# Kernel tuning notes

Measured on AMD Instinct MI355X. Metric: run time of the kernel, lower is better.

The kernel has to match this reference:

```python
import jax, jax.numpy as jnp
import numpy as np

B, S, D_IN, D_OUT, R = 8, 2048, 2048, 2048, 16

def setup_inputs() -> dict:
    key = jax.random.key(0)
    k = jax.random.split(key, 5)
    scale_w = 1.0 / np.sqrt(D_IN)
    return {
        "x": jax.random.normal(k[0], (B, S, D_IN), dtype=jnp.float32),
        "A_params": jax.random.normal(k[1], (B, D_OUT, R), dtype=jnp.float32) * 0.02,
        "B_params": jax.random.normal(k[2], (B, R, D_IN), dtype=jnp.float32) * 0.02,
        "W": jax.random.normal(k[3], (D_OUT, D_IN), dtype=jnp.float32) * scale_w,
        "b": jax.random.normal(k[4], (D_OUT,), dtype=jnp.float32) * scale_w,
    }

def reference(x, A_params, B_params, W, b):
    # base: x @ W^T + b  -> [B, S, out]
    base_out = jnp.einsum("bsi,oi->bso", x, W) + b
    # intermediate = x @ B^T -> [B, S, r]
    intermediate = jnp.einsum("bsi,bri->bsr", x, B_params)
    # adaptation = intermediate @ A^T -> [B, S, out]
    adaptation = jnp.einsum("bsr,bor->bso", intermediate, A_params)
    return base_out + adaptation
```

## Files before the change

### kernel.cpp

```cpp
#include <hip/hip_runtime.h>
#include <cstdint>
#include <cstddef>

typedef __attribute__((ext_vector_type(4))) float  floatx4;
typedef __attribute__((ext_vector_type(8))) __bf16 bf16x8;
typedef __attribute__((ext_vector_type(8))) unsigned short u16x8;

#define M_TOT 16384
#define N_TOT 2048
#define K_TOT 2048
#define NBATCH 8
#define RLORA 16
#define NT 32

__device__ __forceinline__ unsigned short f32_to_bf16(float f) {
  unsigned u = __float_as_uint(f);
  u += 0x7fffu + ((u >> 16) & 1u);
  return (unsigned short)(u >> 16);
}

#define GLOAD_LDS16(gp, lp)                                                        \
  __builtin_amdgcn_global_load_lds((__attribute__((address_space(1))) void*)(void*)(gp), \
                                   (__attribute__((address_space(3))) void*)(void*)(lp), \
                                   16, 0, 0)

template<int V> struct IC { static constexpr int value = V; };

__global__ void k_convert(const float* __restrict__ in, unsigned short* __restrict__ out, int n8) {
  int i = blockIdx.x * blockDim.x + threadIdx.x;
  if (i >= n8) return;
  const float4* p = (const float4*)in + (size_t)i * 2;
  float4 v0 = p[0], v1 = p[1];
  u16x8 o;
  o[0] = f32_to_bf16(v0.x); o[1] = f32_to_bf16(v0.y);
  o[2] = f32_to_bf16(v0.z); o[3] = f32_to_bf16(v0.w);
  o[4] = f32_to_bf16(v1.x); o[5] = f32_to_bf16(v1.y);
  o[6] = f32_to_bf16(v1.z); o[7] = f32_to_bf16(v1.w);
  *(u16x8*)(out + (size_t)i * 8) = o;
}

__global__ void k_convert_a(const float* __restrict__ A, unsigned short* __restrict__ abf) {
  int row = blockIdx.x * blockDim.x + threadIdx.x;
  if (row >= NBATCH * N_TOT) return;
  const float4* p = (const float4*)(A + (size_t)row * RLORA);
  float4 v0 = p[0], v1 = p[1], v2 = p[2], v3 = p[3];
  u16x8 lo, hi2, z = {0,0,0,0,0,0,0,0};
  lo[0] = f32_to_bf16(v0.x); lo[1] = f32_to_bf16(v0.y);
  lo[2] = f32_to_bf16(v0.z); lo[3] = f32_to_bf16(v0.w);
  lo[4] = f32_to_bf16(v1.x); lo[5] = f32_to_bf16(v1.y);
  lo[6] = f32_to_bf16(v1.z); lo[7] = f32_to_bf16(v1.w);
  hi2[0] = f32_to_bf16(v2.x); hi2[1] = f32_to_bf16(v2.y);
  hi2[2] = f32_to_bf16(v2.z); hi2[3] = f32_to_bf16(v2.w);
  hi2[4] = f32_to_bf16(v3.x); hi2[5] = f32_to_bf16(v3.y);
  hi2[6] = f32_to_bf16(v3.z); hi2[7] = f32_to_bf16(v3.w);
  u16x8* dst = (u16x8*)(abf + (size_t)row * 32);
  dst[0] = lo; dst[1] = hi2; dst[2] = z; dst[3] = z;
}

__global__ __launch_bounds__(256) void k_inter(const unsigned short* __restrict__ xbf,
                                               const unsigned short* __restrict__ bpbf,
                                               unsigned short* __restrict__ interbf) {
  const int tid  = threadIdx.x;
  const int lane = tid & 63;
  const int wv   = tid >> 6;
  const int l15  = lane & 15;
  const int hi   = lane >> 4;
  const int m0   = blockIdx.x * 64;
  const int bb   = m0 >> 11;

  floatx4 zero = {0.f, 0.f, 0.f, 0.f};
  floatx4 acc[4] = {zero, zero, zero, zero};

  const unsigned short* bpb = bpbf + (size_t)bb * (RLORA * K_TOT);
  const int kb0 = wv * 512;
  for (int kb = kb0; kb < kb0 + 512; kb += 32) {
    bf16x8 bfr = *(const bf16x8*)(bpb + (size_t)l15 * K_TOT + kb + hi * 8);
    #pragma unroll
    for (int mi = 0; mi < 4; ++mi) {
      bf16x8 afr = *(const bf16x8*)(xbf + (size_t)(m0 + mi * 16 + l15) * K_TOT + kb + hi * 8);
      acc[mi] = __builtin_amdgcn_mfma_f32_16x16x32_bf16(afr, bfr, acc[mi], 0, 0, 0);
    }
  }

  __shared__ floatx4 red[4][4][64];
  #pragma unroll
  for (int mi = 0; mi < 4; ++mi) red[wv][mi][lane] = acc[mi];
  __syncthreads();
  if (wv == 0) {
    #pragma unroll
    for (int mi = 0; mi < 4; ++mi) {
      floatx4 s = red[0][mi][lane] + red[1][mi][lane] + red[2][mi][lane] + red[3][mi][lane];
      #pragma unroll
      for (int j = 0; j < 4; ++j) {
        int m = m0 + mi * 16 + hi * 4 + j;
        interbf[(size_t)m * 32 + l15] = f32_to_bf16(s[j]);
        interbf[(size_t)m * 32 + 16 + l15] = 0;
      }
    }
  }
}

#define STAGE_A(bufi, h, tt) do {                                                      \
  GLOAD_LDS16(Ag + (h)*262144 + (tt)*64 + gOff0, AsB + ((bufi)*2+(h))*16384 + ldsB0);  \
  GLOAD_LDS16(Ag + (h)*262144 + (tt)*64 + gOff1, AsB + ((bufi)*2+(h))*16384 + ldsB1);  \
} while(0)
#define STAGE_B(bufi, h, tt) do {                                                      \
  GLOAD_LDS16(Bg + (h)*262144 + (tt)*64 + gOff0, BsB + ((bufi)*2+(h))*16384 + ldsB0);  \
  GLOAD_LDS16(Bg + (h)*262144 + (tt)*64 + gOff1, BsB + ((bufi)*2+(h))*16384 + ldsB1);  \
} while(0)
#define RDA_(B2, qm, mi, ks) (*(const bf16x8*)(AsB + (B2)*32768 + aBase + (qm)*8192 + (mi)*2048 + koff[ks]))
#define RDB_(B2, ni, ks)     (*(const bf16x8*)(BsB + (B2)*32768 + bBase + (ni)*2048 + koff[ks]))
#define BAR() __builtin_amdgcn_s_barrier()
#define MFMA16(MB, NB, AF, BF) do {                                                        \
  _Pragma("unroll")                                                                        \
  for (int mi = 0; mi < 4; ++mi) {                                                         \
    _Pragma("unroll")                                                                      \
    for (int j = 0; j < 2; ++j) {                                                          \
      acc[(MB)+mi][(NB)+j] = __builtin_amdgcn_mfma_f32_16x16x32_bf16(AF[mi][0], BF[j][0], acc[(MB)+mi][(NB)+j], 0, 0, 0); \
      acc[(MB)+mi][(NB)+j] = __builtin_amdgcn_mfma_f32_16x16x32_bf16(AF[mi][1], BF[j][1], acc[(MB)+mi][(NB)+j], 0, 0, 0); \
    }                                                                                      \
  }                                                                                        \
} while(0)

__global__ __launch_bounds__(512, 2) void k_gemm(const unsigned short* __restrict__ xbf,
                                                 const unsigned short* __restrict__ wbf,
                                                 const unsigned short* __restrict__ interbf,
                                                 const unsigned short* __restrict__ abf,
                                                 const float* __restrict__ bias,
                                                 float* __restrict__ out) {
  __shared__ unsigned short As[2][2][8192];
  __shared__ unsigned short Bs[2][2][8192];
  const int tid  = threadIdx.x;
  const int lane = tid & 63;
  const int wid  = tid >> 6;
  const int wm   = wid >> 2;
  const int wn   = wid & 3;
  const int l15  = lane & 15;
  const int hi   = lane >> 4;
  const int swz  = l15 & 7;

  int bid  = blockIdx.x;
  int swzb = ((bid & 7) << 6) | (bid >> 3);
  const int mt = swzb >> 3;
  const int nt = swzb & 7;
  const int mrow0 = mt << 8;
  const int ncol0 = nt << 8;
  const int bb = mrow0 >> 11;

  const int m0 = mrow0 + wm * 128;
  const int n0 = ncol0 + wn * 64;

  const unsigned short* Ag = xbf + (size_t)mrow0 * K_TOT;
  const unsigned short* Bg = wbf + (size_t)ncol0 * K_TOT;
  char* AsB = (char*)As;
  char* BsB = (char*)Bs;

  const int r0    = tid >> 3;
  const int k80   = (tid & 7) ^ (r0 & 7);
  const int gOff0 = r0 * K_TOT + k80 * 8;
  const int gOff1 = gOff0 + 64 * K_TOT;
  const int ldsB0 = wid * 1024;
  const int ldsB1 = 8192 + wid * 1024;

  const int aBase = wm * 16384 + l15 * 128;
  const int bBase = wn * 8192  + l15 * 128;
  int koff[2];
  koff[0] = ((0 * 4 + hi) ^ swz) * 16;
  koff[1] = ((1 * 4 + hi) ^ swz) * 16;

  floatx4 acc[8][4];
  bf16x8 afA[4][2], afB[4][2], bfP[2][2], bfQ[2][2];

  {
    bf16x8 la[8], lb[4];
    #pragma unroll
    for (int mi = 0; mi < 8; ++mi)
      la[mi] = *(const bf16x8*)(interbf + (size_t)(m0 + mi * 16 + l15) * 32 + hi * 8);
    #pragma unroll
    for (int ni = 0; ni < 4; ++ni)
      lb[ni] = *(const bf16x8*)(abf + ((size_t)bb * N_TOT + n0 + ni * 16 + l15) * 32 + hi * 8);

    STAGE_B(0, 0, 0); STAGE_B(0, 1, 0); STAGE_A(0, 0, 0); STAGE_A(0, 1, 0);
    STAGE_B(1, 0, 1); STAGE_B(1, 1, 1); STAGE_A(1, 0, 1);

    floatx4 z = {0.f, 0.f, 0.f, 0.f};
    #pragma unroll
    for (int mi = 0; mi < 8; ++mi)
      #pragma unroll
      for (int ni = 0; ni < 4; ++ni)
        acc[mi][ni] = __builtin_amdgcn_mfma_f32_16x16x32_bf16(la[mi], lb[ni], z, 0, 0, 0);
  }
  asm volatile("s_waitcnt vmcnt(6)" ::: "memory");
  BAR();
  #pragma unroll
  for (int mi = 0; mi < 4; ++mi) { afA[mi][0] = RDA_(0, 0, mi, 0); afA[mi][1] = RDA_(0, 0, mi, 1); }
  #pragma unroll
  for (int j = 0; j < 2; ++j)    { bfP[j][0]  = RDB_(0, j, 0);     bfP[j][1]  = RDB_(0, j, 1); }

  auto tile_step = [&](int t, auto bufc, auto s1c, auto s2c, auto vmc, auto lastc,
                       auto& bfF, auto& bfS) {
    constexpr int BUF  = decltype(bufc)::value;
    constexpr int S1   = decltype(s1c)::value;
    constexpr int S2   = decltype(s2c)::value;
    constexpr int VM   = decltype(vmc)::value;
    constexpr int LAST = decltype(lastc)::value;

    #pragma unroll
    for (int j = 0; j < 2; ++j) { bfS[j][0] = RDB_(BUF, 2 + j, 0); bfS[j][1] = RDB_(BUF, 2 + j, 1); }
    if constexpr (S1) STAGE_A(BUF ^ 1, 1, t + 1);
    BAR();
    asm volatile("s_waitcnt lgkmcnt(4)" ::: "memory");
    __builtin_amdgcn_s_setprio(1);
    MFMA16(0, 0, afA, bfF);
    __builtin_amdgcn_s_setprio(0);
    BAR();

    #pragma unroll
    for (int mi = 0; mi < 4; ++mi) { afB[mi][0] = RDA_(BUF, 1, mi, 0); afB[mi][1] = RDA_(BUF, 1, mi, 1); }
    BAR();
    asm volatile("s_waitcnt lgkmcnt(8)" ::: "memory");
    __builtin_amdgcn_s_setprio(1);
    MFMA16(0, 2, afA, bfS);
    __builtin_amdgcn_s_setprio(0);
    BAR();

    if constexpr (S2) { STAGE_B(BUF, 0, t + 2); STAGE_B(BUF, 1, t + 2); }
    BAR();
    asm volatile("s_waitcnt lgkmcnt(0)" ::: "memory");
    __builtin_amdgcn_s_setprio(1);
    MFMA16(4, 2, afB, bfS);
    __builtin_amdgcn_s_setprio(0);
    if constexpr (VM == 4)      asm volatile("s_waitcnt vmcnt(4)" ::: "memory");
    else if constexpr (VM == 0) asm volatile("s_waitcnt vmcnt(0)" ::: "memory");
    BAR();

    if constexpr (!LAST) {
      #pragma unroll
      for (int mi = 0; mi < 4; ++mi) { afA[mi][0] = RDA_(BUF ^ 1, 0, mi, 0); afA[mi][1] = RDA_(BUF ^ 1, 0, mi, 1); }
      #pragma unroll
      for (int j = 0; j < 2; ++j)    { bfS[j][0] = RDB_(BUF ^ 1, j, 0);      bfS[j][1] = RDB_(BUF ^ 1, j, 1); }
    }
    if constexpr (S2) STAGE_A(BUF, 0, t + 2);
    BAR();
    __builtin_amdgcn_s_setprio(1);
    MFMA16(4, 0, afB, bfF);
    __builtin_amdgcn_s_setprio(0);
    BAR();
  };

  for (int t = 0; t < NT - 2; t += 2) {
    tile_step(t,     IC<0>{}, IC<1>{}, IC<1>{}, IC<4>{}, IC<0>{}, bfP, bfQ);
    tile_step(t + 1, IC<1>{}, IC<1>{}, IC<1>{}, IC<4>{}, IC<0>{}, bfQ, bfP);
  }
  tile_step(NT - 2, IC<0>{}, IC<1>{}, IC<0>{}, IC<0>{},  IC<0>{}, bfP, bfQ);
  tile_step(NT - 1, IC<1>{}, IC<0>{}, IC<0>{}, IC<-1>{}, IC<1>{}, bfQ, bfP);

  #pragma unroll
  for (int ni = 0; ni < 4; ++ni) {
    int col = n0 + ni * 16 + l15;
    float bv = bias[col];
    #pragma unroll
    for (int mi = 0; mi < 8; ++mi) {
      int r = m0 + mi * 16 + hi * 4;
      #pragma unroll
      for (int j = 0; j < 4; ++j)
        out[(size_t)(r + j) * N_TOT + col] = acc[mi][ni][j] + bv;
    }
  }
}

extern "C" void kernel_launch(void* const* d_in, const int* in_sizes, int n_in,
                              void* d_out, int out_size, void* d_ws, size_t ws_size,
                              hipStream_t stream) {
  const float* x    = (const float*)d_in[0];
  const float* Ap   = (const float*)d_in[1];
  const float* Bp   = (const float*)d_in[2];
  const float* W    = (const float*)d_in[3];
  const float* bias = (const float*)d_in[4];
  float* out = (float*)d_out;

  char* ws = (char*)d_ws;
  unsigned short* xbf     = (unsigned short*)(ws);
  unsigned short* wbf     = (unsigned short*)(ws + 67108864);
  unsigned short* abf     = (unsigned short*)(ws + 67108864 + 8388608);
  unsigned short* bpbf    = (unsigned short*)(ws + 67108864 + 8388608 + 1048576);
  unsigned short* interbf = (unsigned short*)(ws + 67108864 + 8388608 + 1048576 + 524288);

  k_convert<<<dim3(16384), dim3(256), 0, stream>>>(x,  xbf,  4194304);
  k_convert<<<dim3(2048),  dim3(256), 0, stream>>>(W,  wbf,   524288);
  k_convert<<<dim3(128),   dim3(256), 0, stream>>>(Bp, bpbf,   32768);
  k_convert_a<<<dim3(64),  dim3(256), 0, stream>>>(Ap, abf);

  k_inter<<<dim3(256), dim3(256), 0, stream>>>(xbf, bpbf, interbf);

  k_gemm<<<dim3(512), dim3(512), 0, stream>>>(xbf, wbf, interbf, abf, bias, out);
}
```

Measured before the change: 198.8 us.

## Fuse x bf16 conversion into LoRA intermediate kernel and rebalance B-tile prefetch

The separate fp32-to-bf16 conversion passes over x and B_params are folded into the k_inter kernel. It reads fp32 x directly, converts it in registers, feeds the MFMA and writes the bf16 copy for the main GEMM. This removes one full read of x's bf16 copy and two kernel launches. Separately, the main GEMM's tile step now splits the two B-tile global stages and issues the next buffer's B fragment LDS reads earlier, using finer vmcnt waits, to overlap loads with MFMA work. The risk is that k_inter now runs with only 256 blocks while doing the heavy conversion traffic, so bandwidth use may be poor.

```diff
diff --git a/kernel.cpp b/kernel.cpp
--- a/kernel.cpp
+++ b/kernel.cpp
@@ -19,6 +19,15 @@
   return (unsigned short)(u >> 16);
 }
 
+__device__ __forceinline__ u16x8 cvt8(const float4& a, const float4& b) {
+  u16x8 o;
+  o[0] = f32_to_bf16(a.x); o[1] = f32_to_bf16(a.y);
+  o[2] = f32_to_bf16(a.z); o[3] = f32_to_bf16(a.w);
+  o[4] = f32_to_bf16(b.x); o[5] = f32_to_bf16(b.y);
+  o[6] = f32_to_bf16(b.z); o[7] = f32_to_bf16(b.w);
+  return o;
+}
+
 #define GLOAD_LDS16(gp, lp)                                                        \
   __builtin_amdgcn_global_load_lds((__attribute__((address_space(1))) void*)(void*)(gp), \
                                    (__attribute__((address_space(3))) void*)(void*)(lp), \
@@ -30,35 +39,21 @@
   int i = blockIdx.x * blockDim.x + threadIdx.x;
   if (i >= n8) return;
   const float4* p = (const float4*)in + (size_t)i * 2;
-  float4 v0 = p[0], v1 = p[1];
-  u16x8 o;
-  o[0] = f32_to_bf16(v0.x); o[1] = f32_to_bf16(v0.y);
-  o[2] = f32_to_bf16(v0.z); o[3] = f32_to_bf16(v0.w);
-  o[4] = f32_to_bf16(v1.x); o[5] = f32_to_bf16(v1.y);
-  o[6] = f32_to_bf16(v1.z); o[7] = f32_to_bf16(v1.w);
-  *(u16x8*)(out + (size_t)i * 8) = o;
+  *(u16x8*)(out + (size_t)i * 8) = cvt8(p[0], p[1]);
 }
 
 __global__ void k_convert_a(const float* __restrict__ A, unsigned short* __restrict__ abf) {
   int row = blockIdx.x * blockDim.x + threadIdx.x;
   if (row >= NBATCH * N_TOT) return;
   const float4* p = (const float4*)(A + (size_t)row * RLORA);
-  float4 v0 = p[0], v1 = p[1], v2 = p[2], v3 = p[3];
-  u16x8 lo, hi2, z = {0,0,0,0,0,0,0,0};
-  lo[0] = f32_to_bf16(v0.x); lo[1] = f32_to_bf16(v0.y);
-  lo[2] = f32_to_bf16(v0.z); lo[3] = f32_to_bf16(v0.w);
-  lo[4] = f32_to_bf16(v1.x); lo[5] = f32_to_bf16(v1.y);
-  lo[6] = f32_to_bf16(v1.z); lo[7] = f32_to_bf16(v1.w);
-  hi2[0] = f32_to_bf16(v2.x); hi2[1] = f32_to_bf16(v2.y);
-  hi2[2] = f32_to_bf16(v2.z); hi2[3] = f32_to_bf16(v2.w);
-  hi2[4] = f32_to_bf16(v3.x); hi2[5] = f32_to_bf16(v3.y);
-  hi2[6] = f32_to_bf16(v3.z); hi2[7] = f32_to_bf16(v3.w);
+  u16x8 lo = cvt8(p[0], p[1]), hi2 = cvt8(p[2], p[3]), z = {0,0,0,0,0,0,0,0};
   u16x8* dst = (u16x8*)(abf + (size_t)row * 32);
   dst[0] = lo; dst[1] = hi2; dst[2] = z; dst[3] = z;
 }
 
-__global__ __launch_bounds__(256) void k_inter(const unsigned short* __restrict__ xbf,
-                                               const unsigned short* __restrict__ bpbf,
+__global__ __launch_bounds__(256) void k_inter(const float* __restrict__ x,
+                                               const float* __restrict__ Bp,
+                                               unsigned short* __restrict__ xbf,
                                                unsigned short* __restrict__ interbf) {
   const int tid  = threadIdx.x;
   const int lane = tid & 63;
@@ -71,14 +66,19 @@
   floatx4 zero = {0.f, 0.f, 0.f, 0.f};
   floatx4 acc[4] = {zero, zero, zero, zero};
 
-  const unsigned short* bpb = bpbf + (size_t)bb * (RLORA * K_TOT);
+  const float* bpb = Bp + (size_t)bb * (RLORA * K_TOT);
   const int kb0 = wv * 512;
   for (int kb = kb0; kb < kb0 + 512; kb += 32) {
-    bf16x8 bfr = *(const bf16x8*)(bpb + (size_t)l15 * K_TOT + kb + hi * 8);
+    const float* bp = bpb + (size_t)l15 * K_TOT + kb + hi * 8;
+    u16x8 bo = cvt8(*(const float4*)bp, *(const float4*)(bp + 4));
+    bf16x8 bfr = *(bf16x8*)&bo;
     #pragma unroll
     for (int mi = 0; mi < 4; ++mi) {
-      bf16x8 afr = *(const bf16x8*)(xbf + (size_t)(m0 + mi * 16 + l15) * K_TOT + kb + hi * 8);
-      acc[mi] = __builtin_amdgcn_mfma_f32_16x16x32_bf16(afr, bfr, acc[mi], 0, 0, 0);
+      size_t off = (size_t)(m0 + mi * 16 + l15) * K_TOT + kb + hi * 8;
+      const float* xp = x + off;
+      u16x8 ao = cvt8(*(const float4*)xp, *(const float4*)(xp + 4));
+      *(u16x8*)(xbf + off) = ao;
+      acc[mi] = __builtin_amdgcn_mfma_f32_16x16x32_bf16(*(bf16x8*)&ao, bfr, acc[mi], 0, 0, 0);
     }
   }
 
@@ -169,7 +169,7 @@
   koff[1] = ((1 * 4 + hi) ^ swz) * 16;
 
   floatx4 acc[8][4];
-  bf16x8 afA[4][2], afB[4][2], bfP[2][2], bfQ[2][2];
+  bf16x8 afA[4][2], afB[4][2], bfS[2][2], bfP[2][2], bfQ[2][2];
 
   {
     bf16x8 la[8], lb[4];
@@ -197,12 +197,13 @@
   #pragma unroll
   for (int j = 0; j < 2; ++j)    { bfP[j][0]  = RDB_(0, j, 0);     bfP[j][1]  = RDB_(0, j, 1); }
 
-  auto tile_step = [&](int t, auto bufc, auto s1c, auto s2c, auto vmc, auto lastc,
-                       auto& bfF, auto& bfS) {
+  auto tile_step = [&](int t, auto bufc, auto s1c, auto s2c, auto vm3c, auto vm4c, auto lastc,
+                       auto& bfF, auto& bfN) {
     constexpr int BUF  = decltype(bufc)::value;
     constexpr int S1   = decltype(s1c)::value;
     constexpr int S2   = decltype(s2c)::value;
-    constexpr int VM   = decltype(vmc)::value;
+    constexpr int VM3  = decltype(vm3c)::value;
+    constexpr int VM4  = decltype(vm4c)::value;
     constexpr int LAST = decltype(lastc)::value;
 
     #pragma unroll
@@ -217,6 +218,7 @@
 
     #pragma unroll
     for (int mi = 0; mi < 4; ++mi) { afB[mi][0] = RDA_(BUF, 1, mi, 0); afB[mi][1] = RDA_(BUF, 1, mi, 1); }
+    if constexpr (S2) STAGE_B(BUF, 0, t + 2);
     BAR();
     asm volatile("s_waitcnt lgkmcnt(8)" ::: "memory");
     __builtin_amdgcn_s_setprio(1);
@@ -224,21 +226,31 @@
     __builtin_amdgcn_s_setprio(0);
     BAR();
 
-    if constexpr (S2) { STAGE_B(BUF, 0, t + 2); STAGE_B(BUF, 1, t + 2); }
-    BAR();
-    asm volatile("s_waitcnt lgkmcnt(0)" ::: "memory");
+    if constexpr (VM3 >= 0) {
+      if constexpr (VM3 == 6)      asm volatile("s_waitcnt vmcnt(6)" ::: "memory");
+      else if constexpr (VM3 == 4) asm volatile("s_waitcnt vmcnt(4)" ::: "memory");
+      else                         asm volatile("s_waitcnt vmcnt(0)" ::: "memory");
+    }
+    if constexpr (!LAST) {
+      #pragma unroll
+      for (int j = 0; j < 2; ++j) { bfN[j][0] = RDB_(BUF ^ 1, j, 0); bfN[j][1] = RDB_(BUF ^ 1, j, 1); }
+    }
+    if constexpr (S2) STAGE_B(BUF, 1, t + 2);
+    BAR();
+    if constexpr (LAST) asm volatile("s_waitcnt lgkmcnt(0)" ::: "memory");
+    else                asm volatile("s_waitcnt lgkmcnt(4)" ::: "memory");
     __builtin_amdgcn_s_setprio(1);
     MFMA16(4, 2, afB, bfS);
     __builtin_amdgcn_s_setprio(0);
-    if constexpr (VM == 4)      asm volatile("s_waitcnt vmcnt(4)" ::: "memory");
-    else if constexpr (VM == 0) asm volatile("s_waitcnt vmcnt(0)" ::: "memory");
-    BAR();
-
+    BAR();
+
+    if constexpr (VM4 >= 0) {
+      if constexpr (VM4 == 4) asm volatile("s_waitcnt vmcnt(4)" ::: "memory");
+      else                    asm volatile("s_waitcnt vmcnt(0)" ::: "memory");
+    }
     if constexpr (!LAST) {
       #pragma unroll
       for (int mi = 0; mi < 4; ++mi) { afA[mi][0] = RDA_(BUF ^ 1, 0, mi, 0); afA[mi][1] = RDA_(BUF ^ 1, 0, mi, 1); }
-      #pragma unroll
-      for (int j = 0; j < 2; ++j)    { bfS[j][0] = RDB_(BUF ^ 1, j, 0);      bfS[j][1] = RDB_(BUF ^ 1, j, 1); }
     }
     if constexpr (S2) STAGE_A(BUF, 0, t + 2);
     BAR();
@@ -249,11 +261,11 @@
   };
 
   for (int t = 0; t < NT - 2; t += 2) {
-    tile_step(t,     IC<0>{}, IC<1>{}, IC<1>{}, IC<4>{}, IC<0>{}, bfP, bfQ);
-    tile_step(t + 1, IC<1>{}, IC<1>{}, IC<1>{}, IC<4>{}, IC<0>{}, bfQ, bfP);
-  }
-  tile_step(NT - 2, IC<0>{}, IC<1>{}, IC<0>{}, IC<0>{},  IC<0>{}, bfP, bfQ);
-  tile_step(NT - 1, IC<1>{}, IC<0>{}, IC<0>{}, IC<-1>{}, IC<1>{}, bfQ, bfP);
+    tile_step(t,     IC<0>{}, IC<1>{}, IC<1>{}, IC<6>{}, IC<4>{}, IC<0>{}, bfP, bfQ);
+    tile_step(t + 1, IC<1>{}, IC<1>{}, IC<1>{}, IC<6>{}, IC<4>{}, IC<0>{}, bfQ, bfP);
+  }
+  tile_step(NT - 2, IC<0>{}, IC<1>{}, IC<0>{}, IC<4>{}, IC<0>{},  IC<0>{}, bfP, bfQ);
+  tile_step(NT - 1, IC<1>{}, IC<0>{}, IC<0>{}, IC<-1>{}, IC<-1>{}, IC<1>{}, bfQ, bfP);
 
   #pragma unroll
   for (int ni = 0; ni < 4; ++ni) {
@@ -283,15 +295,12 @@
   unsigned short* xbf     = (unsigned short*)(ws);
   unsigned short* wbf     = (unsigned short*)(ws + 67108864);
   unsigned short* abf     = (unsigned short*)(ws + 67108864 + 8388608);
-  unsigned short* bpbf    = (unsigned short*)(ws + 67108864 + 8388608 + 1048576);
-  unsigned short* interbf = (unsigned short*)(ws + 67108864 + 8388608 + 1048576 + 524288);
-
-  k_convert<<<dim3(16384), dim3(256), 0, stream>>>(x,  xbf,  4194304);
-  k_convert<<<dim3(2048),  dim3(256), 0, stream>>>(W,  wbf,   524288);
-  k_convert<<<dim3(128),   dim3(256), 0, stream>>>(Bp, bpbf,   32768);
+  unsigned short* interbf = (unsigned short*)(ws + 67108864 + 8388608 + 1048576);
+
+  k_convert<<<dim3(2048),  dim3(256), 0, stream>>>(W,  wbf, 524288);
   k_convert_a<<<dim3(64),  dim3(256), 0, stream>>>(Ap, abf);
 
-  k_inter<<<dim3(256), dim3(256), 0, stream>>>(xbf, bpbf, interbf);
+  k_inter<<<dim3(256), dim3(256), 0, stream>>>(x, Bp, xbf, interbf);
 
   k_gemm<<<dim3(512), dim3(512), 0, stream>>>(xbf, wbf, interbf, abf, bias, out);
 }
```

After: 246.8 us. 1.24x slower.
